# Optimization experiments

Measured on AMD Instinct MI355X. Metric: run time of the kernel, lower is better.

Reference implementation:

```python
import jax, jax.numpy as jnp
import numpy as np

# Model dims (see shape_source)
N, S, E, NMP, H, O = 20000, 16, 160000, 2, 4, 64
D_FEAT, E_DIM, PREP, NCLS, B = 64, 32, 128, 8, 4096
D1 = H * O  # 256, node/edge dim after layer 0


def setup_inputs() -> dict:
    key = jax.random.key(0)
    ks = jax.random.split(key, 24)
    g = lambda i, shape, fan: jax.random.normal(ks[i], shape, jnp.float32) * (fan ** -0.5)
    return {
        "feats": jax.random.normal(ks[0], (N, D_FEAT), jnp.float32),
        "edge_emb": jax.random.normal(ks[1], (NMP, E, E_DIM), jnp.float32),
        "W_prep0": g(2, (D_FEAT, PREP), D_FEAT),
        "W_prep1": g(3, (D_FEAT, PREP), D_FEAT),
        "edge_prep_w": g(4, (NMP, E_DIM, PREP), E_DIM),
        "edge_wq_l0": g(5, (NMP, H, PREP, O), PREP),
        "edge_wk_l0": g(6, (NMP, H, PREP, O), PREP),
        "edge_wq_l1": g(7, (NMP, H, D1, O), D1),
        "edge_wk_l1": g(8, (NMP, H, D1, O), D1),
        "node_wq_l0": g(9, (NMP, H, PREP, O), PREP),
        "node_wk_l0": g(10, (NMP, H, PREP, O), PREP),
        "node_wq_l1": g(11, (NMP, H, D1, O), D1),
        "node_wk_l1": g(12, (NMP, H, D1, O), D1),
        "Wg": g(13, (2 * D1, PREP), 2 * D1),
        "vg": g(14, (PREP,), PREP),
        "W_fc": g(15, (2 * D1, NCLS), 2 * D1),
        "b_fc": jnp.zeros((NCLS,), jnp.float32),
        "node2edge_idx": jax.random.randint(ks[20], (NMP, N, S), 0, E),
        "edge_node_adj": jax.random.randint(ks[21], (NMP, E, 2), 0, N),
        "train_ids": jax.random.randint(ks[22], (B,), 0, N),
    }


def _attn_agg(x_q, x_neigh, wq, wk):
    """Multi-head attention aggregator.
    x_q [M,d], x_neigh [M,s,d2], wq [H,d,O], wk [H,d2,O] -> [M, H*O]."""
    q = jnp.einsum('md,hdo->mho', x_q, wq)
    k = jnp.einsum('msd,hdo->msho', x_neigh, wk)
    logits = jnp.einsum('mho,msho->mhs', q, k) / np.float32(np.sqrt(O))
    a = jax.nn.softmax(logits, axis=-1)
    agg = jnp.einsum('mhs,msho->mho', a, k)
    out = jax.nn.elu(q + agg)
    return out.reshape(out.shape[0], H * O)


def reference(feats, edge_emb, W_prep0, W_prep1, edge_prep_w,
              edge_wq_l0, edge_wk_l0, edge_wq_l1, edge_wk_l1,
              node_wq_l0, node_wk_l0, node_wq_l1, node_wk_l1,
              Wg, vg, W_fc, b_fc,
              node2edge_idx, edge_node_adj, train_ids):
    e_wq, e_wk = [edge_wq_l0, edge_wq_l1], [edge_wk_l0, edge_wk_l1]
    n_wq, n_wk = [node_wq_l0, node_wq_l1], [node_wk_l0, node_wk_l1]
    outs = []
    for mp in range(NMP):  # small fixed count of message-passing branches
        dummy = feats @ W_prep0          # prep layer 0  [N,PREP]
        all_feats = feats @ W_prep1      # prep layer 1  [N,PREP]
        all_edges = edge_emb[mp] @ edge_prep_w[mp]  # [E,PREP]
        skip = []
        for l in range(2):  # depth
            # edge update: gather endpoint node feats [E,2,d], attend, concat heads
            neigh_nodes = all_feats[edge_node_adj[mp]]
            next_edges = _attn_agg(all_edges, neigh_nodes, e_wq[l][mp], e_wk[l][mp])
            # node update: gather incident edge feats [N,S,d] from OLD all_edges
            src = dummy if l == 0 else all_feats
            neigh_edges = all_edges[node2edge_idx[mp]]
            next_feats = _attn_agg(src, neigh_edges, n_wq[l][mp], n_wk[l][mp])
            skip.append(next_feats)
            all_feats, all_edges = next_feats, next_edges
        outs.append(jnp.concatenate(skip, axis=-1)[train_ids])  # [B, 2*D1]
    x = jnp.stack(outs, 0)  # [NMP, B, 512]
    # gated metapath aggregation (mp_agg): softmax over mp axis
    gate = jax.nn.softmax(jnp.einsum('mbe,e->mb', jnp.tanh(jnp.einsum('mbd,de->mbe', x, Wg)), vg), axis=0)
    pooled = jnp.einsum('mb,mbd->bd', gate, x)
    logits = pooled @ W_fc + b_fc  # [B, NCLS]
    return logits, gate
```

## Files before the change

### kernel.cpp

```cpp
#include <hip/hip_runtime.h>
#include <hip/hip_bf16.h>
#include <math.h>

#define N_NODES 20000
#define S_NE    16
#define E_EDGES 160000
#define NMP     2
#define H_HEADS 4
#define O_DIM   64
#define D_FEAT  64
#define E_DIMC  32
#define PREP    128
#define NCLS    8
#define B_TR    4096
#define D1      256
#define NSLOT   (B_TR * S_NE)

#define LDA0    132
#define LDA1    260
#define NPAD    264

typedef __hip_bfloat16 bf16;
typedef unsigned short u16;
typedef __attribute__((ext_vector_type(8))) short s8v;
typedef __attribute__((ext_vector_type(4))) float f4v;

template <typename T>
__device__ __forceinline__ float ldv(const void* p, size_t i) {
    if constexpr (sizeof(T) == 4) return ((const float*)p)[i];
    else return __bfloat162float(((const bf16*)p)[i]);
}
template <typename T>
__device__ __forceinline__ float4 ld4(const void* p, size_t i) {
    if constexpr (sizeof(T) == 4) {
        return *(const float4*)((const float*)p + i);
    } else {
        float4 r;
        r.x = ldv<T>(p, i); r.y = ldv<T>(p, i + 1);
        r.z = ldv<T>(p, i + 2); r.w = ldv<T>(p, i + 3);
        return r;
    }
}
template <typename T>
__device__ __forceinline__ void stv(void* p, size_t i, float v) {
    if constexpr (sizeof(T) == 4) ((float*)p)[i] = v;
    else ((bf16*)p)[i] = __float2bfloat16(v);
}
template <typename T>
__device__ __forceinline__ bool active(const int* flag) {
    return *flag == (sizeof(T) == 4 ? 1 : 0);
}

__device__ __forceinline__ u16 f2bf(float x) {
    bf16 h = __float2bfloat16(x);
    return *reinterpret_cast<u16*>(&h);
}
__device__ __forceinline__ float bf2f(u16 u) {
    bf16 h; *reinterpret_cast<u16*>(&h) = u;
    return __bfloat162float(h);
}
__device__ __forceinline__ void splitbf(float x, u16& h, u16& l) {
    h = f2bf(x);
    l = f2bf(x - bf2f(h));
}

__device__ __forceinline__ float wave_sum(float v) {
    #pragma unroll
    for (int off = 32; off > 0; off >>= 1) v += __shfl_xor(v, off, 64);
    return v;
}
__device__ __forceinline__ float og_sum(float v) {
    v += __shfl_xor(v, 4, 64);  v += __shfl_xor(v, 8, 64);
    v += __shfl_xor(v, 16, 64); v += __shfl_xor(v, 32, 64);
    return v;
}
__device__ __forceinline__ float grp16_sum(float v) {
    v += __shfl_xor(v, 1, 64); v += __shfl_xor(v, 2, 64);
    v += __shfl_xor(v, 4, 64); v += __shfl_xor(v, 8, 64);
    return v;
}
__device__ __forceinline__ float mg_sum(float v) {
    v += __shfl_xor(v, 1, 64); v += __shfl_xor(v, 2, 64); return v;
}
__device__ __forceinline__ float mg_max(float v) {
    v = fmaxf(v, __shfl_xor(v, 1, 64)); v = fmaxf(v, __shfl_xor(v, 2, 64)); return v;
}
__device__ __forceinline__ float eluf(float x) { return x > 0.f ? x : expf(x) - 1.f; }
__device__ __forceinline__ float4 elu4(float4 v) {
    v.x = eluf(v.x); v.y = eluf(v.y); v.z = eluf(v.z); v.w = eluf(v.w); return v;
}

#define FMA4C(acc, s, b) do { (acc).x += (s)*(b).x; (acc).y += (s)*(b).y; \
                              (acc).z += (s)*(b).z; (acc).w += (s)*(b).w; } while (0)
#define ZERO4(v) do { (v).x = 0.f; (v).y = 0.f; (v).z = 0.f; (v).w = 0.f; } while (0)

__global__ void k_detect(const unsigned* __restrict__ w, int* __restrict__ flag) {
    int t = threadIdx.x;
    int bad = 0;
    for (int i = t; i < 512; i += 64) {
        float v = __uint_as_float((w[i] & 0xffffu) << 16);
        if (!(fabsf(v) < 64.f)) bad++;
    }
    #pragma unroll
    for (int off = 32; off > 0; off >>= 1) bad += __shfl_xor(bad, off, 64);
    if (t == 0) *flag = (bad > 32) ? 1 : 0;
}

template <typename T>
__device__ void precomb2_body(const void* epw, const void* ewq, const void* nwk0,
                              const void* Wp1, const void* ewk,
                              const void* Wp0, const void* nwq0,
                              float* wkn, float* wq0,
                              u16* qeh, u16* qel, u16* k0h, u16* k0l) {
    int idx = blockIdx.x * 256 + threadIdx.x;
    if (idx >= 98304) return;
    int combo, rem;
    if (idx < 16384)      { combo = 0; rem = idx; }
    else if (idx < 32768) { combo = 1; rem = idx - 16384; }
    else if (idx < 65536) { combo = 2; rem = idx - 32768; }
    else                  { combo = 3; rem = idx - 65536; }
    int mp, r, n;
    if (combo < 2) { mp = rem >> 13; r = (rem >> 8) & 31; n = rem & 255; }
    else           { mp = rem >> 14; r = (rem >> 8) & 63; n = rem & 255; }
    int h = n >> 6, o = n & 63;
    const void* Aw; const void* Bw; size_t aoff;
    size_t boff = (size_t)mp * H_HEADS * PREP * O_DIM + (size_t)h * PREP * O_DIM + o;
    switch (combo) {
        case 0: Aw = epw; Bw = ewq;  aoff = (size_t)mp * E_DIMC * PREP + (size_t)r * PREP; break;
        case 1: Aw = epw; Bw = nwk0; aoff = (size_t)mp * E_DIMC * PREP + (size_t)r * PREP; break;
        case 2: Aw = Wp1; Bw = ewk;  aoff = (size_t)r * PREP; break;
        default:Aw = Wp0; Bw = nwq0; aoff = (size_t)r * PREP; break;
    }
    float acc = 0.f;
    #pragma unroll 4
    for (int p = 0; p < PREP; ++p)
        acc += ldv<T>(Aw, aoff + p) * ldv<T>(Bw, boff + (size_t)p * O_DIM);
    if (combo < 2) {
        u16 hh, ll; splitbf(acc, hh, ll);
        size_t dst = (size_t)mp * (256 * 32) + (size_t)n * 32 + r;
        if (combo == 0) { qeh[dst] = hh; qel[dst] = ll; }
        else            { k0h[dst] = hh; k0l[dst] = ll; }
    } else if (combo == 2) {
        wkn[(size_t)mp * 64 * D1 + (size_t)r * D1 + n] = acc;
    } else {
        wq0[(size_t)mp * 64 * D1 + (size_t)r * D1 + n] = acc;
    }
}
__global__ void k_precomb2(const void* epw, const void* ewq, const void* nwk0,
                           const void* Wp1, const void* ewk,
                           const void* Wp0, const void* nwq0,
                           float* wkn, float* wq0,
                           u16* qeh, u16* qel, u16* k0h, u16* k0l,
                           const int* flag) {
    if (*flag == 1) precomb2_body<float>(epw, ewq, nwk0, Wp1, ewk, Wp0, nwq0, wkn, wq0, qeh, qel, k0h, k0l);
    else            precomb2_body<bf16 >(epw, ewq, nwk0, Wp1, ewk, Wp0, nwq0, wkn, wq0, qeh, qel, k0h, k0l);
}

template <typename T>
__device__ void embsplit_body(const void* emb, u16* eh, u16* el) {
    size_t idx = (size_t)blockIdx.x * 256 + threadIdx.x;
    if (idx >= (size_t)NMP * E_EDGES * E_DIMC) return;
    float v = ldv<T>(emb, idx);
    u16 hh, ll; splitbf(v, hh, ll);
    eh[idx] = hh; el[idx] = ll;
}
__global__ void k_embsplit(const void* emb, u16* eh, u16* el, const int* flag) {
    if (*flag == 1) embsplit_body<float>(emb, eh, el);
    else            embsplit_body<bf16 >(emb, eh, el);
}

template <typename T>
__device__ void wt1_body(const void* wk1, const void* wq1,
                         u16* kth, u16* ktl, u16* qth, u16* qtl) {
    int idx = blockIdx.x * 256 + threadIdx.x;
    int k = idx & 255, n = (idx >> 8) & 255;
    int wsel = (idx >> 16) & 1, mp = idx >> 17;
    size_t src = (size_t)mp * (H_HEADS * D1 * O_DIM) + (size_t)(n >> 6) * (D1 * O_DIM)
               + (size_t)k * O_DIM + (n & 63);
    float v = ldv<T>(wsel ? wq1 : wk1, src);
    u16 h, l; splitbf(v, h, l);
    size_t dst = (size_t)mp * 65536 + (size_t)n * 256 + k;
    if (wsel) { qth[dst] = h; qtl[dst] = l; }
    else      { kth[dst] = h; ktl[dst] = l; }
}
__global__ void k_wt1(const void* wk1, const void* wq1,
                      u16* kth, u16* ktl, u16* qth, u16* qtl, const int* flag) {
    if (*flag == 1) wt1_body<float>(wk1, wq1, kth, ktl, qth, qtl);
    else            wt1_body<bf16 >(wk1, wq1, kth, ktl, qth, qtl);
}

template <typename T>
__device__ void wgt_body(const void* Wg, u16* gh, u16* gl) {
    int idx = blockIdx.x * 256 + threadIdx.x;
    int n = idx >> 9, k = idx & 511;
    float v = ldv<T>(Wg, (size_t)k * PREP + n);
    u16 h, l; splitbf(v, h, l);
    gh[(size_t)n * 512 + k] = h;
    gl[(size_t)n * 512 + k] = l;
}
__global__ void k_wgt(const void* Wg, u16* gh, u16* gl, const int* flag) {
    if (*flag == 1) wgt_body<float>(Wg, gh, gl);
    else            wgt_body<bf16 >(Wg, gh, gl);
}

template <typename TA, typename TB>
__device__ void gemm_body(const void* A, size_t aOff, const int* Aidx, int strideA,
                          const void* B, int sH, int sD,
                          float* C, int ldC, int M, int K) {
    int bm = blockIdx.x * 64;
    int h  = blockIdx.y;
    int t  = threadIdx.x;
    int tx = t & 15, ty = t >> 4;

    __shared__ float As[32][68];
    __shared__ float Bs[32][68];

    float acc[4][4] = {{0.f}};
    int arow = t >> 3, kq = (t & 7) * 4;
    int brow = t >> 4, nq = (t & 15) * 4;

    for (int k0 = 0; k0 < K; k0 += 32) {
        #pragma unroll
        for (int c = 0; c < 2; ++c) {
            int rm = arow + 32 * c;
            int gr = bm + rm;
            gr = (gr < M) ? gr : 0;
            size_t row = Aidx ? (size_t)Aidx[gr] : (size_t)gr;
            float4 a = ld4<TA>(A, aOff + row * strideA + k0 + kq);
            As[kq + 0][rm] = a.x; As[kq + 1][rm] = a.y;
            As[kq + 2][rm] = a.z; As[kq + 3][rm] = a.w;
        }
        #pragma unroll
        for (int c = 0; c < 2; ++c) {
            int rk = brow + 16 * c;
            float4 b = ld4<TB>(B, (size_t)h * sH + (size_t)(k0 + rk) * sD + nq);
            *(float4*)&Bs[rk][nq] = b;
        }
        __syncthreads();
        #pragma unroll
        for (int kk = 0; kk < 32; ++kk) {
            float4 av = *(const float4*)&As[kk][ty * 4];
            float4 bv = *(const float4*)&Bs[kk][tx * 4];
            float am[4] = {av.x, av.y, av.z, av.w};
            #pragma unroll
            for (int i = 0; i < 4; ++i) {
                acc[i][0] += am[i] * bv.x; acc[i][1] += am[i] * bv.y;
                acc[i][2] += am[i] * bv.z; acc[i][3] += am[i] * bv.w;
            }
        }
        __syncthreads();
    }
    #pragma unroll
    for (int i = 0; i < 4; ++i) {
        int m = bm + ty * 4 + i;
        if (m < M) {
            float4 st; st.x = acc[i][0]; st.y = acc[i][1];
            st.z = acc[i][2]; st.w = acc[i][3];
            *(float4*)&C[(size_t)m * ldC + h * 64 + tx * 4] = st;
        }
    }
}
__global__ __launch_bounds__(256) void k_gemm_rf(
        const void* A, size_t aOff, const int* Aidx, int strideA,
        const float* B, int sH, int sD, float* C, int ldC, int M, int K,
        const int* flag) {
    if (*flag == 1) gemm_body<float, float>(A, aOff, Aidx, strideA, B, sH, sD, C, ldC, M, K);
    else            gemm_body<bf16,  float>(A, aOff, Aidx, strideA, B, sH, sD, C, ldC, M, K);
}

template <int K, bool G>
__device__ __forceinline__ void mfma_core(
        const u16* __restrict__ Ah, const u16* __restrict__ Al,
        const int* __restrict__ rows,
        const u16* __restrict__ Bh, const u16* __restrict__ Bl,
        int rbase, int bn, int lane, f4v acc[4][4]) {
    int fr = lane & 15;
    int kq = (lane >> 4) * 8;
    #pragma unroll
    for (int i = 0; i < 4; ++i)
        #pragma unroll
        for (int j = 0; j < 4; ++j) acc[i][j] = f4v{0.f, 0.f, 0.f, 0.f};
    #pragma unroll 2
    for (int k0 = 0; k0 < K; k0 += 32) {
        s8v ah[4], al[4], bh[4], bl[4];
        #pragma unroll
        for (int i = 0; i < 4; ++i) {
            size_t arow;
            if constexpr (G) arow = (size_t)rows[rbase + i * 16 + fr];
            else             arow = (size_t)(rbase + i * 16 + fr);
            size_t ao = arow * K + k0 + kq;
            ah[i] = *(const s8v*)(Ah + ao);
            al[i] = *(const s8v*)(Al + ao);
            size_t bo = (size_t)(bn + i * 16 + fr) * K + k0 + kq;
            bh[i] = *(const s8v*)(Bh + bo);
            bl[i] = *(const s8v*)(Bl + bo);
        }
        #pragma unroll
        for (int i = 0; i < 4; ++i)
            #pragma unroll
            for (int j = 0; j < 4; ++j) {
                acc[i][j] = __builtin_amdgcn_mfma_f32_16x16x32_bf16(al[i], bh[j], acc[i][j], 0, 0, 0);
                acc[i][j] = __builtin_amdgcn_mfma_f32_16x16x32_bf16(ah[i], bl[j], acc[i][j], 0, 0, 0);
                acc[i][j] = __builtin_amdgcn_mfma_f32_16x16x32_bf16(ah[i], bh[j], acc[i][j], 0, 0, 0);
            }
    }
}

template <int K>
__global__ __launch_bounds__(256) void k_mfma(
        const u16* __restrict__ Ah, const u16* __restrict__ Al,
        const u16* __restrict__ Bh, const u16* __restrict__ Bl,
        float* __restrict__ C, int ldC) {
    int w = threadIdx.x >> 6, lane = threadIdx.x & 63;
    int bm = blockIdx.x * 128 + (w & 1) * 64;
    int bn = blockIdx.y * 128 + (w >> 1) * 64;
    f4v acc[4][4];
    mfma_core<K, false>(Ah, Al, nullptr, Bh, Bl, bm, bn, lane, acc);
    int cn = lane & 15, cr = (lane >> 4) * 4;
    #pragma unroll
    for (int i = 0; i < 4; ++i) {
        int m0 = bm + i * 16 + cr;
        #pragma unroll
        for (int j = 0; j < 4; ++j) {
            int n = bn + j * 16 + cn;
            #pragma unroll
            for (int r = 0; r < 4; ++r)
                C[(size_t)(m0 + r) * ldC + n] = acc[i][j][r];
        }
    }
}

template <int K, bool G>
__global__ __launch_bounds__(256) void k_mfma_nattn(
        const u16* __restrict__ Ah, const u16* __restrict__ Al,
        const int* __restrict__ rows,
        const u16* __restrict__ Bh, const u16* __restrict__ Bl,
        const float* __restrict__ q,
        u16* __restrict__ o0h, u16* __restrict__ o0l,
        float* __restrict__ xrow, int xoff,
        u16* __restrict__ xh, u16* __restrict__ xl) {
    int w = threadIdx.x >> 6, lane = threadIdx.x & 63;
    int rbase = blockIdx.x * 128 + (w & 1) * 64;
    int bn = blockIdx.y * 128 + (w >> 1) * 64;
    f4v acc[4][4];
    mfma_core<K, G>(Ah, Al, rows, Bh, Bl, rbase, bn, lane, acc);

    int cn = lane & 15, grp = lane >> 4;
    #pragma unroll
    for (int i = 0; i < 4; ++i) {
        int b = (rbase >> 4) + i;
        float qv[4];
        #pragma unroll
        for (int j = 0; j < 4; ++j)
            qv[j] = q[(size_t)b * D1 + bn + j * 16 + cn];
        float lg[4];
        #pragma unroll
        for (int r = 0; r < 4; ++r) {
            float p = 0.f;
            #pragma unroll
            for (int j = 0; j < 4; ++j) p += acc[i][j][r] * qv[j];
            lg[r] = grp16_sum(p) * 0.125f;
        }
        float mx = fmaxf(fmaxf(lg[0], lg[1]), fmaxf(lg[2], lg[3]));
        mx = fmaxf(mx, __shfl_xor(mx, 16, 64));
        mx = fmaxf(mx, __shfl_xor(mx, 32, 64));
        float e[4], s = 0.f;
        #pragma unroll
        for (int r = 0; r < 4; ++r) { e[r] = expf(lg[r] - mx); s += e[r]; }
        s += __shfl_xor(s, 16, 64);
        s += __shfl_xor(s, 32, 64);
        float inv = 1.f / s;
        #pragma unroll
        for (int j = 0; j < 4; ++j) {
            float ag = e[0] * acc[i][j][0] + e[1] * acc[i][j][1]
                     + e[2] * acc[i][j][2] + e[3] * acc[i][j][3];
            ag += __shfl_xor(ag, 16, 64);
            ag += __shfl_xor(ag, 32, 64);
            float v = eluf(qv[j] + ag * inv);
            if (grp == 0) {
                int col = bn + j * 16 + cn;
                xrow[(size_t)b * (2 * D1) + xoff + col] = v;
                u16 hh, ll; splitbf(v, hh, ll);
                xh[(size_t)b * (2 * D1) + xoff + col] = hh;
                xl[(size_t)b * (2 * D1) + xoff + col] = ll;
                if (o0h) {
                    o0h[(size_t)b * D1 + col] = hh;
                    o0l[(size_t)b * D1 + col] = ll;
                }
            }
        }
    }
}

__global__ __launch_bounds__(256) void k_mega(
        const u16* __restrict__ Ah, const u16* __restrict__ Al,
        const int* __restrict__ rows,
        const u16* __restrict__ qBh, const u16* __restrict__ qBl,
        const float* __restrict__ Kn,
        const int* __restrict__ adjA, const int* __restrict__ adjB,
        const u16* __restrict__ kBh, const u16* __restrict__ kBl,
        const float* __restrict__ q,
        float* __restrict__ xrow,
        u16* __restrict__ xh, u16* __restrict__ xl) {
    __shared__ u16 sh_[64][NPAD];
    __shared__ u16 sl_[64][NPAD];
    int w = threadIdx.x >> 6, lane = threadIdx.x & 63;
    int rbase = blockIdx.x * 64;
    int bn = w * 64;

    f4v acc[4][4];
    mfma_core<32, true>(Ah, Al, rows, qBh, qBl, rbase, bn, lane, acc);

    int cn = lane & 15, cr = (lane >> 4) * 4;
    #pragma unroll
    for (int i = 0; i < 4; ++i) {
        #pragma unroll
        for (int r = 0; r < 4; ++r) {
            int lrow = i * 16 + cr + r;
            int slot = rbase + lrow;
            size_t ra = (size_t)adjA[slot] * D1;
            size_t rb = (size_t)adjB[slot] * D1;
            float kA[4], kB[4];
            float pA = 0.f, pB = 0.f;
            #pragma unroll
            for (int j = 0; j < 4; ++j) {
                int col = bn + j * 16 + cn;
                kA[j] = Kn[ra + col];
                kB[j] = Kn[rb + col];
                pA += acc[i][j][r] * kA[j];
                pB += acc[i][j][r] * kB[j];
            }
            float lA = grp16_sum(pA) * 0.125f;
            float lB = grp16_sum(pB) * 0.125f;
            float m = fmaxf(lA, lB);
            float eA = expf(lA - m), eB = expf(lB - m);
            float inv = 1.f / (eA + eB);
            #pragma unroll
            for (int j = 0; j < 4; ++j) {
                int col = bn + j * 16 + cn;
                float v = eluf(acc[i][j][r] + (eA * kA[j] + eB * kB[j]) * inv);
                u16 hh, ll; splitbf(v, hh, ll);
                sh_[lrow][col] = hh;
                sl_[lrow][col] = ll;
            }
        }
    }
    __syncthreads();

    int fr = lane & 15, kq = (lane >> 4) * 8;
    #pragma unroll
    for (int i = 0; i < 4; ++i)
        #pragma unroll
        for (int j = 0; j < 4; ++j) acc[i][j] = f4v{0.f, 0.f, 0.f, 0.f};
    #pragma unroll 2
    for (int k0 = 0; k0 < 256; k0 += 32) {
        s8v ah[4], al[4], bh[4], bl[4];
        #pragma unroll
        for (int i = 0; i < 4; ++i) {
            int lr = i * 16 + fr;
            ah[i] = *(const s8v*)&sh_[lr][k0 + kq];
            al[i] = *(const s8v*)&sl_[lr][k0 + kq];
            size_t bo = (size_t)(bn + i * 16 + fr) * 256 + k0 + kq;
            bh[i] = *(const s8v*)(kBh + bo);
            bl[i] = *(const s8v*)(kBl + bo);
        }
        #pragma unroll
        for (int i = 0; i < 4; ++i)
            #pragma unroll
            for (int j = 0; j < 4; ++j) {
                acc[i][j] = __builtin_amdgcn_mfma_f32_16x16x32_bf16(al[i], bh[j], acc[i][j], 0, 0, 0);
                acc[i][j] = __builtin_amdgcn_mfma_f32_16x16x32_bf16(ah[i], bl[j], acc[i][j], 0, 0, 0);
                acc[i][j] = __builtin_amdgcn_mfma_f32_16x16x32_bf16(ah[i], bh[j], acc[i][j], 0, 0, 0);
            }
    }

    int grp = lane >> 4;
    #pragma unroll
    for (int i = 0; i < 4; ++i) {
        int b = (rbase >> 4) + i;
        float qv[4];
        #pragma unroll
        for (int j = 0; j < 4; ++j)
            qv[j] = q[(size_t)b * D1 + bn + j * 16 + cn];
        float lg[4];
        #pragma unroll
        for (int r = 0; r < 4; ++r) {
            float p = 0.f;
            #pragma unroll
            for (int j = 0; j < 4; ++j) p += acc[i][j][r] * qv[j];
            lg[r] = grp16_sum(p) * 0.125f;
        }
        float mx = fmaxf(fmaxf(lg[0], lg[1]), fmaxf(lg[2], lg[3]));
        mx = fmaxf(mx, __shfl_xor(mx, 16, 64));
        mx = fmaxf(mx, __shfl_xor(mx, 32, 64));
        float e[4], s = 0.f;
        #pragma unroll
        for (int r = 0; r < 4; ++r) { e[r] = expf(lg[r] - mx); s += e[r]; }
        s += __shfl_xor(s, 16, 64);
        s += __shfl_xor(s, 32, 64);
        float inv = 1.f / s;
        #pragma unroll
        for (int j = 0; j < 4; ++j) {
            float ag = e[0] * acc[i][j][0] + e[1] * acc[i][j][1]
                     + e[2] * acc[i][j][2] + e[3] * acc[i][j][3];
            ag += __shfl_xor(ag, 16, 64);
            ag += __shfl_xor(ag, 32, 64);
            float v = eluf(qv[j] + ag * inv);
            if (grp == 0) {
                int col = bn + j * 16 + cn;
                xrow[(size_t)b * (2 * D1) + D1 + col] = v;
                u16 hh, ll; splitbf(v, hh, ll);
                xh[(size_t)b * (2 * D1) + D1 + col] = hh;
                xl[(size_t)b * (2 * D1) + D1 + col] = ll;
            }
        }
    }
}

__global__ void k_slot_setup(const int* __restrict__ n2e_mp,
                             const int* __restrict__ adj_mp,
                             const int* __restrict__ tid,
                             int* __restrict__ eid,
                             int* __restrict__ adjA,
                             int* __restrict__ adjB) {
    int i = blockIdx.x * blockDim.x + threadIdx.x;
    if (i >= NSLOT) return;
    int b = i >> 4, s = i & 15;
    int e = n2e_mp[(size_t)tid[b] * S_NE + s];
    eid[i] = e;
    adjA[i] = adj_mp[(size_t)e * 2 + 0];
    adjB[i] = adj_mp[(size_t)e * 2 + 1];
}

template <typename T>
__device__ void gate_fin_body(const float* gmat, const void* vg, float* gate_pre) {
    int row = blockIdx.x;
    int t = threadIdx.x;
    float v = tanhf(gmat[(size_t)row * PREP + t]) * ldv<T>(vg, t);
    __shared__ float red[128];
    red[t] = v;
    __syncthreads();
    for (int s = 64; s > 0; s >>= 1) { if (t < s) red[t] += red[t + s]; __syncthreads(); }
    if (t == 0) gate_pre[row] = red[0];
}
__global__ void k_gate_fin(const float* gmat, const void* vg, float* gate_pre,
                           const int* flag) {
    if (*flag == 1) gate_fin_body<float>(gmat, vg, gate_pre);
    else            gate_fin_body<bf16 >(gmat, vg, gate_pre);
}

template <typename T>
__device__ void gate_dir_body(const float* xcat, const void* Wg, const void* vg,
                              float* gate_pre) {
    int mb = blockIdx.x;
    int t = threadIdx.x;
    __shared__ float xr[2 * D1];
    for (int idx = t; idx < 2 * D1; idx += 128) xr[idx] = xcat[(size_t)mb * (2 * D1) + idx];
    __syncthreads();
    float acc = 0.f;
    for (int d = 0; d < 2 * D1; ++d) acc += xr[d] * ldv<T>(Wg, (size_t)d * PREP + t);
    float gp = tanhf(acc) * ldv<T>(vg, t);
    __shared__ float red[128];
    red[t] = gp;
    __syncthreads();
    for (int s = 64; s > 0; s >>= 1) { if (t < s) red[t] += red[t + s]; __syncthreads(); }
    if (t == 0) gate_pre[mb] = red[0];
}
__global__ void k_gate_direct(const float* xcat, const void* Wg, const void* vg,
                              float* gate_pre, const int* flag) {
    if (*flag == 1) gate_dir_body<float>(xcat, Wg, vg, gate_pre);
    else            gate_dir_body<bf16 >(xcat, Wg, vg, gate_pre);
}

template <typename T>
__device__ void final_body(const float* xcat, const float* gate_pre,
                           const void* Wfc, const void* bfc, void* out) {
    int b = blockIdx.x;
    int t = threadIdx.x;
    float g0 = gate_pre[b], g1 = gate_pre[B_TR + b];
    float mx = fmaxf(g0, g1);
    float e0 = expf(g0 - mx), e1 = expf(g1 - mx);
    float inv = 1.f / (e0 + e1);
    float w0 = e0 * inv, w1 = e1 * inv;
    __shared__ float pooled[2 * D1];
    for (int d = t; d < 2 * D1; d += 64)
        pooled[d] = w0 * xcat[(size_t)b * (2 * D1) + d]
                  + w1 * xcat[(size_t)(B_TR + b) * (2 * D1) + d];
    __syncthreads();
    if (t < NCLS) {
        float acc = ldv<T>(bfc, t);
        for (int d = 0; d < 2 * D1; ++d) acc += pooled[d] * ldv<T>(Wfc, (size_t)d * NCLS + t);
        stv<T>(out, (size_t)b * NCLS + t, acc);
    }
    if (t == 8) stv<T>(out, (size_t)B_TR * NCLS + b, w0);
    if (t == 9) stv<T>(out, (size_t)B_TR * NCLS + B_TR + b, w1);
}
__global__ void k_final(const float* xcat, const float* gate_pre,
                        const void* Wfc, const void* bfc, void* out,
                        const int* flag) {
    if (*flag == 1) final_body<float>(xcat, gate_pre, Wfc, bfc, out);
    else            final_body<bf16 >(xcat, gate_pre, Wfc, bfc, out);
}

template <typename T>
__global__ void k_prep_nodes(const void* __restrict__ feats,
                             const void* __restrict__ W,
                             float* __restrict__ out,
                             const int* __restrict__ flag) {
    if (!active<T>(flag)) return;
    int g = blockIdx.x * blockDim.x + threadIdx.x;
    if (g >= N_NODES * 32) return;
    int n = g >> 5, pg = g & 31;
    float4 acc; ZERO4(acc);
    #pragma unroll 8
    for (int d = 0; d < D_FEAT; ++d) {
        float f = ldv<T>(feats, (size_t)n * D_FEAT + d);
        float4 w4 = ld4<T>(W, (size_t)d * PREP + pg * 4);
        FMA4C(acc, f, w4);
    }
    *(float4*)(out + (size_t)n * PREP + pg * 4) = acc;
}

template <typename T>
__global__ __launch_bounds__(256) void k_fused(
        const void* __restrict__ feats,
        const void* __restrict__ edge_emb_mp,
        const void* __restrict__ W_prep0,
        const void* __restrict__ epw_mp,
        const void* __restrict__ ewq,
        const void* __restrict__ ewk,
        const void* __restrict__ nwq0,
        const void* __restrict__ nwk0,
        const void* __restrict__ nwq1,
        const void* __restrict__ nwk1,
        const int*  __restrict__ n2e_mp,
        const int*  __restrict__ adj_mp,
        const int*  __restrict__ tid,
        const float* __restrict__ all_feats0,
        float* __restrict__ xcat_mp,
        const int* __restrict__ flag) {
    if (!active<T>(flag)) return;
    int b = blockIdx.x;
    int t = threadIdx.x;
    int h = t >> 6;
    int lane = t & 63;
    int mg = lane & 3, og = lane >> 2;

    __shared__ int   s_eid[S_NE];
    __shared__ int   s_nrow[2 * S_NE];
    __shared__ __align__(16) float s_emb[S_NE * E_DIMC];
    __shared__ __align__(16) float s_f[D_FEAT];
    __shared__ __align__(16) float s_q0[PREP];
    __shared__ __align__(16) float s_eprep[S_NE * LDA0];
    __shared__ __align__(16) float s_xn_pool[2 * S_NE * LDA0];
    __shared__ __align__(16) float s_out0[D1];
    float* s_nedge = s_xn_pool;

    int tid_b = tid[b];
    if (t < S_NE)   s_eid[t] = n2e_mp[(size_t)tid_b * S_NE + t];
    if (t < D_FEAT) s_f[t] = ldv<T>(feats, (size_t)tid_b * D_FEAT + t);
    __syncthreads();

    if (t < 2 * S_NE) s_nrow[t] = adj_mp[(size_t)s_eid[t >> 1] * 2 + (t & 1)];
    {
        int j = t, s = j >> 5, d = j & 31;
        s_emb[j] = ldv<T>(edge_emb_mp, (size_t)s_eid[s] * E_DIMC + d);
        j = t + 256; s = j >> 5; d = j & 31;
        s_emb[j] = ldv<T>(edge_emb_mp, (size_t)s_eid[s] * E_DIMC + d);
    }
    if (t < PREP) {
        float a = 0.f;
        #pragma unroll
        for (int d = 0; d < D_FEAT; ++d) a += s_f[d] * ldv<T>(W_prep0, d * PREP + t);
        s_q0[t] = a;
    }
    __syncthreads();

    #pragma unroll
    for (int k = 0; k < 4; ++k) {
        int j = t + 256 * k;
        int r = j >> 5, dc = j & 31;
        float4 v = *(const float4*)(all_feats0 + (size_t)s_nrow[r] * PREP + dc * 4);
        *(float4*)&s_xn_pool[r * LDA0 + dc * 4] = v;
    }
    {
        int s = t >> 4, pg = t & 15;
        float4 a0, a1; ZERO4(a0); ZERO4(a1);
        #pragma unroll
        for (int d = 0; d < E_DIMC; ++d) {
            float e = s_emb[s * E_DIMC + d];
            float4 w0 = ld4<T>(epw_mp, (size_t)d * PREP + pg * 8);
            float4 w1 = ld4<T>(epw_mp, (size_t)d * PREP + pg * 8 + 4);
            FMA4C(a0, e, w0); FMA4C(a1, e, w1);
        }
        *(float4*)&s_eprep[s * LDA0 + pg * 8]     = a0;
        *(float4*)&s_eprep[s * LDA0 + pg * 8 + 4] = a1;
    }
    __syncthreads();

    float4 aq[4], ak[8];
    #pragma unroll
    for (int i = 0; i < 4; ++i) ZERO4(aq[i]);
    #pragma unroll
    for (int i = 0; i < 8; ++i) ZERO4(ak[i]);
    {
        size_t wb = (size_t)h * PREP * O_DIM + og * 4;
        for (int kk = 0; kk < PREP; kk += 4) {
            float4 bq[4], bk[4];
            #pragma unroll
            for (int j = 0; j < 4; ++j) {
                bq[j] = ld4<T>(ewq, wb + (size_t)(kk + j) * O_DIM);
                bk[j] = ld4<T>(ewk, wb + (size_t)(kk + j) * O_DIM);
            }
            #pragma unroll
            for (int i = 0; i < 4; ++i) {
                float4 a = *(const float4*)&s_eprep[(mg + 4 * i) * LDA0 + kk];
                FMA4C(aq[i], a.x, bq[0]); FMA4C(aq[i], a.y, bq[1]);
                FMA4C(aq[i], a.z, bq[2]); FMA4C(aq[i], a.w, bq[3]);
            }
            #pragma unroll
            for (int i = 0; i < 8; ++i) {
                int r = 2 * mg + (i & 1) + 8 * (i >> 1);
                float4 a = *(const float4*)&s_xn_pool[r * LDA0 + kk];
                FMA4C(ak[i], a.x, bk[0]); FMA4C(ak[i], a.y, bk[1]);
                FMA4C(ak[i], a.z, bk[2]); FMA4C(ak[i], a.w, bk[3]);
            }
        }
    }
    __syncthreads();

    #pragma unroll
    for (int j = 0; j < 4; ++j) {
        int s = mg + 4 * j;
        float4 q = aq[j], kA = ak[2 * j], kB = ak[2 * j + 1];
        float lA = og_sum(q.x * kA.x + q.y * kA.y + q.z * kA.z + q.w * kA.w) * 0.125f;
        float lB = og_sum(q.x * kB.x + q.y * kB.y + q.z * kB.z + q.w * kB.w) * 0.125f;
        float m = fmaxf(lA, lB);
        float eA = expf(lA - m), eB = expf(lB - m);
        float inv = 1.f / (eA + eB);
        float4 v;
        v.x = q.x + (eA * kA.x + eB * kB.x) * inv;
        v.y = q.y + (eA * kA.y + eB * kB.y) * inv;
        v.z = q.z + (eA * kA.z + eB * kB.z) * inv;
        v.w = q.w + (eA * kA.w + eB * kB.w) * inv;
        *(float4*)&s_nedge[s * LDA1 + h * O_DIM + og * 4] = elu4(v);
    }

    float4 zq; ZERO4(zq);
    float4 zk[4];
    #pragma unroll
    for (int i = 0; i < 4; ++i) ZERO4(zk[i]);
    {
        size_t wb = (size_t)h * PREP * O_DIM + og * 4;
        for (int kk = 0; kk < PREP; kk += 4) {
            float4 q4 = *(const float4*)&s_q0[kk];
            float4 bq[4], bk[4];
            #pragma unroll
            for (int j = 0; j < 4; ++j) {
                bq[j] = ld4<T>(nwq0, wb + (size_t)(kk + j) * O_DIM);
                bk[j] = ld4<T>(nwk0, wb + (size_t)(kk + j) * O_DIM);
            }
            FMA4C(zq, q4.x, bq[0]); FMA4C(zq, q4.y, bq[1]);
            FMA4C(zq, q4.z, bq[2]); FMA4C(zq, q4.w, bq[3]);
            #pragma unroll
            for (int i = 0; i < 4; ++i) {
                float4 a = *(const float4*)&s_eprep[(mg + 4 * i) * LDA0 + kk];
                FMA4C(zk[i], a.x, bk[0]); FMA4C(zk[i], a.y, bk[1]);
                FMA4C(zk[i], a.z, bk[2]); FMA4C(zk[i], a.w, bk[3]);
            }
        }
    }
    {
        float lg[4];
        #pragma unroll
        for (int j = 0; j < 4; ++j)
            lg[j] = og_sum(zq.x * zk[j].x + zq.y * zk[j].y +
                           zq.z * zk[j].z + zq.w * zk[j].w) * 0.125f;
        float mx = fmaxf(fmaxf(lg[0], lg[1]), fmaxf(lg[2], lg[3]));
        mx = mg_max(mx);
        float ea[4], ssum = 0.f;
        #pragma unroll
        for (int j = 0; j < 4; ++j) { ea[j] = expf(lg[j] - mx); ssum += ea[j]; }
        ssum = mg_sum(ssum);
        float inv = 1.f / ssum;
        float4 part; ZERO4(part);
        #pragma unroll
        for (int j = 0; j < 4; ++j) FMA4C(part, ea[j], zk[j]);
        part.x = mg_sum(part.x); part.y = mg_sum(part.y);
        part.z = mg_sum(part.z); part.w = mg_sum(part.w);
        float4 v;
        v.x = zq.x + part.x * inv; v.y = zq.y + part.y * inv;
        v.z = zq.z + part.z * inv; v.w = zq.w + part.w * inv;
        v = elu4(v);
        if (mg == 0) {
            *(float4*)&s_out0[h * O_DIM + og * 4] = v;
            *(float4*)(xcat_mp + (size_t)b * (2 * D1) + h * O_DIM + og * 4) = v;
        }
    }
    __syncthreads();

    ZERO4(zq);
    #pragma unroll
    for (int i = 0; i < 4; ++i) ZERO4(zk[i]);
    {
        size_t wb = (size_t)h * D1 * O_DIM + og * 4;
        for (int kk = 0; kk < D1; kk += 4) {
            float4 q4 = *(const float4*)&s_out0[kk];
            float4 bq[4], bk[4];
            #pragma unroll
            for (int j = 0; j < 4; ++j) {
                bq[j] = ld4<T>(nwq1, wb + (size_t)(kk + j) * O_DIM);
                bk[j] = ld4<T>(nwk1, wb + (size_t)(kk + j) * O_DIM);
            }
            FMA4C(zq, q4.x, bq[0]); FMA4C(zq, q4.y, bq[1]);
            FMA4C(zq, q4.z, bq[2]); FMA4C(zq, q4.w, bq[3]);
            #pragma unroll
            for (int i = 0; i < 4; ++i) {
                float4 a = *(const float4*)&s_nedge[(mg + 4 * i) * LDA1 + kk];
                FMA4C(zk[i], a.x, bk[0]); FMA4C(zk[i], a.y, bk[1]);
                FMA4C(zk[i], a.z, bk[2]); FMA4C(zk[i], a.w, bk[3]);
            }
        }
    }
    {
        float lg[4];
        #pragma unroll
        for (int j = 0; j < 4; ++j)
            lg[j] = og_sum(zq.x * zk[j].x + zq.y * zk[j].y +
                           zq.z * zk[j].z + zq.w * zk[j].w) * 0.125f;
        float mx = fmaxf(fmaxf(lg[0], lg[1]), fmaxf(lg[2], lg[3]));
        mx = mg_max(mx);
        float ea[4], ssum = 0.f;
        #pragma unroll
        for (int j = 0; j < 4; ++j) { ea[j] = expf(lg[j] - mx); ssum += ea[j]; }
        ssum = mg_sum(ssum);
        float inv = 1.f / ssum;
        float4 part; ZERO4(part);
        #pragma unroll
        for (int j = 0; j < 4; ++j) FMA4C(part, ea[j], zk[j]);
        part.x = mg_sum(part.x); part.y = mg_sum(part.y);
        part.z = mg_sum(part.z); part.w = mg_sum(part.w);
        float4 v;
        v.x = zq.x + part.x * inv; v.y = zq.y + part.y * inv;
        v.z = zq.z + part.z * inv; v.w = zq.w + part.w * inv;
        v = elu4(v);
        if (mg == 0)
            *(float4*)(xcat_mp + (size_t)b * (2 * D1) + D1 + h * O_DIM + og * 4) = v;
    }
}

extern "C" void kernel_launch(void* const* d_in, const int* in_sizes, int n_in,
                              void* d_out, int out_size, void* d_ws, size_t ws_size,
                              hipStream_t stream) {
    const void* feats       = d_in[0];
    const void* edge_emb    = d_in[1];
    const void* W_prep0     = d_in[2];
    const void* W_prep1     = d_in[3];
    const void* edge_prep_w = d_in[4];
    const void* e_wq0       = d_in[5];
    const void* e_wk0       = d_in[6];
    const void* n_wq0       = d_in[9];
    const void* n_wk0       = d_in[10];
    const void* n_wq1       = d_in[11];
    const void* n_wk1       = d_in[12];
    const void* Wg          = d_in[13];
    const void* vg          = d_in[14];
    const void* Wfc         = d_in[15];
    const void* bfc         = d_in[16];
    const int*  n2e         = (const int*)d_in[17];
    const int*  adj         = (const int*)d_in[18];
    const int*  tid         = (const int*)d_in[19];

    float* ws   = (float*)d_ws;
    int*   flag = (int*)ws;
    float* base = ws + 4;
    size_t avail = (ws_size >= 16) ? (ws_size - 16) / 4 : 0;

    k_detect<<<1, 64, 0, stream>>>((const unsigned*)feats, flag);

    size_t off = 0;
    auto alloc = [&](size_t n) { size_t o = off; off += (n + 3) & ~(size_t)3; return o; };
    size_t o_xcat = alloc((size_t)NMP * B_TR * 2 * D1);
    size_t o_gmat = alloc((size_t)NMP * B_TR * PREP);
    size_t o_gpre = alloc(NMP * B_TR);
    size_t o_wkn  = alloc(NMP * 64 * D1);
    size_t o_wq0  = alloc(NMP * 64 * D1);
    size_t o_qeh  = alloc(NMP * 256 * 32 / 2);
    size_t o_qel  = alloc(NMP * 256 * 32 / 2);
    size_t o_k0h  = alloc(NMP * 256 * 32 / 2);
    size_t o_k0l  = alloc(NMP * 256 * 32 / 2);
    size_t o_ebh  = alloc((size_t)NMP * E_EDGES * E_DIMC / 2);
    size_t o_ebl  = alloc((size_t)NMP * E_EDGES * E_DIMC / 2);
    size_t o_Kn   = alloc((size_t)N_NODES * D1);
    size_t o_q0   = alloc((size_t)B_TR * D1);
    size_t o_Q1   = alloc((size_t)B_TR * D1);
    size_t o_eid  = alloc(NSLOT);
    size_t o_adjA = alloc(NSLOT);
    size_t o_adjB = alloc(NSLOT);
    size_t o_o0h  = alloc((size_t)B_TR * D1 / 2);
    size_t o_o0l  = alloc((size_t)B_TR * D1 / 2);
    size_t o_xh   = alloc((size_t)NMP * B_TR * D1);
    size_t o_xl   = alloc((size_t)NMP * B_TR * D1);
    size_t o_wk1h = alloc((size_t)NMP * 32768);
    size_t o_wk1l = alloc((size_t)NMP * 32768);
    size_t o_wq1h = alloc((size_t)NMP * 32768);
    size_t o_wq1l = alloc((size_t)NMP * 32768);
    size_t o_wgh  = alloc(32768);
    size_t o_wgl  = alloc(32768);
    size_t fixed = off;

    int CH = (fixed <= avail) ? B_TR : 0;

    if (CH > 0) {
        float* xcat = base + o_xcat;
        float* gmat = base + o_gmat;
        float* gpre = base + o_gpre;
        float* wkn  = base + o_wkn;
        float* wq0  = base + o_wq0;
        u16*   qeh  = (u16*)(base + o_qeh);
        u16*   qel  = (u16*)(base + o_qel);
        u16*   k0h  = (u16*)(base + o_k0h);
        u16*   k0l  = (u16*)(base + o_k0l);
        u16*   ebh  = (u16*)(base + o_ebh);
        u16*   ebl  = (u16*)(base + o_ebl);
        float* Kn   = base + o_Kn;
        float* q0   = base + o_q0;
        float* Q1   = base + o_Q1;
        int*   eid  = (int*)(base + o_eid);
        int*   adjA = (int*)(base + o_adjA);
        int*   adjB = (int*)(base + o_adjB);
        u16*   o0h  = (u16*)(base + o_o0h);
        u16*   o0l  = (u16*)(base + o_o0l);
        u16*   xh   = (u16*)(base + o_xh);
        u16*   xl   = (u16*)(base + o_xl);
        u16*   wk1h = (u16*)(base + o_wk1h);
        u16*   wk1l = (u16*)(base + o_wk1l);
        u16*   wq1h = (u16*)(base + o_wq1h);
        u16*   wq1l = (u16*)(base + o_wq1l);
        u16*   wgh  = (u16*)(base + o_wgh);
        u16*   wgl  = (u16*)(base + o_wgl);
        int NC = B_TR / CH;

        k_precomb2<<<384, 256, 0, stream>>>(edge_prep_w, e_wq0, n_wk0, W_prep1,
                                            e_wk0, W_prep0, n_wq0,
                                            wkn, wq0, qeh, qel, k0h, k0l, flag);
        k_embsplit<<<(NMP * E_EDGES * E_DIMC + 255) / 256, 256, 0, stream>>>(
            edge_emb, ebh, ebl, flag);
        k_wt1<<<1024, 256, 0, stream>>>(n_wk1, n_wq1, wk1h, wk1l, wq1h, wq1l, flag);
        k_wgt<<<256, 256, 0, stream>>>(Wg, wgh, wgl, flag);

        for (int mp = 0; mp < NMP; ++mp) {
            k_slot_setup<<<(NSLOT + 255) / 256, 256, 0, stream>>>(
                n2e + (size_t)mp * N_NODES * S_NE,
                adj + (size_t)mp * E_EDGES * 2,
                tid, eid, adjA, adjB);

            k_gemm_rf<<<dim3((N_NODES + 63) / 64, 4), 256, 0, stream>>>(
                feats, 0, nullptr, D_FEAT, wkn + (size_t)mp * 64 * D1,
                64, D1, Kn, D1, N_NODES, D_FEAT, flag);
            k_gemm_rf<<<dim3(B_TR / 64, 4), 256, 0, stream>>>(
                feats, 0, tid, D_FEAT, wq0 + (size_t)mp * 64 * D1,
                64, D1, q0, D1, B_TR, D_FEAT, flag);

            const u16* ebh_mp = ebh + (size_t)mp * E_EDGES * E_DIMC;
            const u16* ebl_mp = ebl + (size_t)mp * E_EDGES * E_DIMC;

            for (int c = 0; c < NC; ++c) {
                int c0 = c * CH;
                int MS = CH * S_NE;
                k_mfma_nattn<32, true><<<dim3(MS / 128, 2), 256, 0, stream>>>(
                    ebh_mp, ebl_mp, eid + (size_t)c0 * S_NE,
                    k0h + (size_t)mp * 8192, k0l + (size_t)mp * 8192,
                    q0 + (size_t)c0 * D1, o0h, o0l,
                    xcat + ((size_t)mp * B_TR + c0) * 2 * D1, 0,
                    xh + ((size_t)mp * B_TR + c0) * 2 * D1,
                    xl + ((size_t)mp * B_TR + c0) * 2 * D1);
                k_mfma<256><<<dim3(CH / 128, 2), 256, 0, stream>>>(
                    o0h, o0l, wq1h + (size_t)mp * 65536, wq1l + (size_t)mp * 65536,
                    Q1, D1);
                k_mega<<<MS / 64, 256, 0, stream>>>(
                    ebh_mp, ebl_mp, eid + (size_t)c0 * S_NE,
                    qeh + (size_t)mp * 8192, qel + (size_t)mp * 8192,
                    Kn, adjA + (size_t)c0 * S_NE, adjB + (size_t)c0 * S_NE,
                    wk1h + (size_t)mp * 65536, wk1l + (size_t)mp * 65536,
                    Q1,
                    xcat + ((size_t)mp * B_TR + c0) * 2 * D1,
                    xh + ((size_t)mp * B_TR + c0) * 2 * D1,
                    xl + ((size_t)mp * B_TR + c0) * 2 * D1);
            }
        }
        k_mfma<512><<<dim3(NMP * B_TR / 128, 1), 256, 0, stream>>>(
            xh, xl, wgh, wgl, gmat, PREP);
        k_gate_fin<<<NMP * B_TR, 128, 0, stream>>>(gmat, vg, gpre, flag);
        k_final<<<B_TR, 64, 0, stream>>>(xcat, gpre, Wfc, bfc, d_out, flag);
    } else {
        size_t f_off = 0;
        auto falloc = [&](size_t n) { size_t o = f_off; f_off += (n + 3) & ~(size_t)3; return o; };
        float* af0  = base + falloc((size_t)N_NODES * PREP);
        float* xcat = base + falloc((size_t)NMP * B_TR * 2 * D1);
        float* gpre = base + falloc(NMP * B_TR);

        k_prep_nodes<float><<<(N_NODES * 32 + 255) / 256, 256, 0, stream>>>(
            feats, W_prep1, af0, flag);
        k_prep_nodes<bf16><<<(N_NODES * 32 + 255) / 256, 256, 0, stream>>>(
            feats, W_prep1, af0, flag);

        for (int mp = 0; mp < NMP; ++mp) {
            #define FUSED_ARGS(esz)                                                   \
                feats,                                                                \
                (const char*)edge_emb + (esz) * (size_t)mp * E_EDGES * E_DIMC,        \
                W_prep0,                                                              \
                (const char*)edge_prep_w + (esz) * (size_t)mp * E_DIMC * PREP,        \
                (const char*)e_wq0 + (esz) * (size_t)mp * H_HEADS * PREP * O_DIM,     \
                (const char*)e_wk0 + (esz) * (size_t)mp * H_HEADS * PREP * O_DIM,     \
                (const char*)n_wq0 + (esz) * (size_t)mp * H_HEADS * PREP * O_DIM,     \
                (const char*)n_wk0 + (esz) * (size_t)mp * H_HEADS * PREP * O_DIM,     \
                (const char*)n_wq1 + (esz) * (size_t)mp * H_HEADS * D1 * O_DIM,       \
                (const char*)n_wk1 + (esz) * (size_t)mp * H_HEADS * D1 * O_DIM,       \
                n2e + (size_t)mp * N_NODES * S_NE,                                    \
                adj + (size_t)mp * E_EDGES * 2,                                       \
                tid, af0, xcat + (size_t)mp * B_TR * 2 * D1, flag
            k_fused<float><<<B_TR, 256, 0, stream>>>(FUSED_ARGS(4));
            k_fused<bf16><<<B_TR, 256, 0, stream>>>(FUSED_ARGS(2));
            #undef FUSED_ARGS
        }
        k_gate_direct<<<NMP * B_TR, 128, 0, stream>>>(xcat, Wg, vg, gpre, flag);
        k_final<<<B_TR, 64, 0, stream>>>(xcat, gpre, Wfc, bfc, d_out, flag);
    }
}
```

Measured before the change: 513.9 us.

## Split k_mega across 8 waves with 32-row tiles and inline first GEMM

k_mega now launches 512 threads per block, so each wave handles a 32x64 tile instead of a 64x64 tile. The accumulator array shrinks from 4x4 to 2x4, and the first GEMM is inlined instead of calling mfma_core. Adjacency indices are loaded before the MFMA so their latency can overlap with the matrix work. The aim is lower register pressure and more waves in flight to hide the gather latency, at the cost of each wave reloading the B operand for its half of the rows.

```diff
diff --git a/kernel.cpp b/kernel.cpp
--- a/kernel.cpp
+++ b/kernel.cpp
@@ -392,7 +392,7 @@
     }
 }
 
-__global__ __launch_bounds__(256) void k_mega(
+__global__ __launch_bounds__(512, 4) void k_mega(
         const u16* __restrict__ Ah, const u16* __restrict__ Al,
         const int* __restrict__ rows,
         const u16* __restrict__ qBh, const u16* __restrict__ qBl,
@@ -405,21 +405,59 @@
     __shared__ u16 sh_[64][NPAD];
     __shared__ u16 sl_[64][NPAD];
     int w = threadIdx.x >> 6, lane = threadIdx.x & 63;
-    int rbase = blockIdx.x * 64;
-    int bn = w * 64;
-
-    f4v acc[4][4];
-    mfma_core<32, true>(Ah, Al, rows, qBh, qBl, rbase, bn, lane, acc);
-
+    int wr = w & 1, wc = w >> 1;
+    int blk = blockIdx.x * 64;
+    int rbase = blk + wr * 32;
+    int bn = wc * 64;
+    int fr = lane & 15, kq = (lane >> 4) * 8;
     int cn = lane & 15, cr = (lane >> 4) * 4;
-    #pragma unroll
-    for (int i = 0; i < 4; ++i) {
+
+    int raA[2][4], raB[2][4];
+    #pragma unroll
+    for (int i = 0; i < 2; ++i)
         #pragma unroll
         for (int r = 0; r < 4; ++r) {
-            int lrow = i * 16 + cr + r;
-            int slot = rbase + lrow;
-            size_t ra = (size_t)adjA[slot] * D1;
-            size_t rb = (size_t)adjB[slot] * D1;
+            int slot = rbase + i * 16 + cr + r;
+            raA[i][r] = adjA[slot] * D1;
+            raB[i][r] = adjB[slot] * D1;
+        }
+
+    f4v acc[2][4];
+    #pragma unroll
+    for (int i = 0; i < 2; ++i)
+        #pragma unroll
+        for (int j = 0; j < 4; ++j) acc[i][j] = f4v{0.f, 0.f, 0.f, 0.f};
+    {
+        s8v ah[2], al[2], bh[4], bl[4];
+        #pragma unroll
+        for (int i = 0; i < 2; ++i) {
+            size_t ao = (size_t)rows[rbase + i * 16 + fr] * E_DIMC + kq;
+            ah[i] = *(const s8v*)(Ah + ao);
+            al[i] = *(const s8v*)(Al + ao);
+        }
+        #pragma unroll
+        for (int j = 0; j < 4; ++j) {
+            size_t bo = (size_t)(bn + j * 16 + fr) * E_DIMC + kq;
+            bh[j] = *(const s8v*)(qBh + bo);
+            bl[j] = *(const s8v*)(qBl + bo);
+        }
+        #pragma unroll
+        for (int i = 0; i < 2; ++i)
+            #pragma unroll
+            for (int j = 0; j < 4; ++j) {
+                acc[i][j] = __builtin_amdgcn_mfma_f32_16x16x32_bf16(al[i], bh[j], acc[i][j], 0, 0, 0);
+                acc[i][j] = __builtin_amdgcn_mfma_f32_16x16x32_bf16(ah[i], bl[j], acc[i][j], 0, 0, 0);
+                acc[i][j] = __builtin_amdgcn_mfma_f32_16x16x32_bf16(ah[i], bh[j], acc[i][j], 0, 0, 0);
+            }
+    }
+
+    #pragma unroll
+    for (int i = 0; i < 2; ++i) {
+        #pragma unroll
+        for (int r = 0; r < 4; ++r) {
+            int lrow = wr * 32 + i * 16 + cr + r;
+            size_t ra = (size_t)raA[i][r];
+            size_t rb = (size_t)raB[i][r];
             float kA[4], kB[4];
             float pA = 0.f, pB = 0.f;
             #pragma unroll
@@ -447,25 +485,27 @@
     }
     __syncthreads();
 
-    int fr = lane & 15, kq = (lane >> 4) * 8;
-    #pragma unroll
-    for (int i = 0; i < 4; ++i)
+    #pragma unroll
+    for (int i = 0; i < 2; ++i)
         #pragma unroll
         for (int j = 0; j < 4; ++j) acc[i][j] = f4v{0.f, 0.f, 0.f, 0.f};
     #pragma unroll 2
     for (int k0 = 0; k0 < 256; k0 += 32) {
-        s8v ah[4], al[4], bh[4], bl[4];
-        #pragma unroll
-        for (int i = 0; i < 4; ++i) {
-            int lr = i * 16 + fr;
+        s8v ah[2], al[2], bh[4], bl[4];
+        #pragma unroll
+        for (int i = 0; i < 2; ++i) {
+            int lr = wr * 32 + i * 16 + fr;
             ah[i] = *(const s8v*)&sh_[lr][k0 + kq];
             al[i] = *(const s8v*)&sl_[lr][k0 + kq];
-            size_t bo = (size_t)(bn + i * 16 + fr) * 256 + k0 + kq;
-            bh[i] = *(const s8v*)(kBh + bo);
-            bl[i] = *(const s8v*)(kBl + bo);
-        }
-        #pragma unroll
-        for (int i = 0; i < 4; ++i)
+        }
+        #pragma unroll
+        for (int j = 0; j < 4; ++j) {
+            size_t bo = (size_t)(bn + j * 16 + fr) * 256 + k0 + kq;
+            bh[j] = *(const s8v*)(kBh + bo);
+            bl[j] = *(const s8v*)(kBl + bo);
+        }
+        #pragma unroll
+        for (int i = 0; i < 2; ++i)
             #pragma unroll
             for (int j = 0; j < 4; ++j) {
                 acc[i][j] = __builtin_amdgcn_mfma_f32_16x16x32_bf16(al[i], bh[j], acc[i][j], 0, 0, 0);
@@ -476,7 +516,7 @@
 
     int grp = lane >> 4;
     #pragma unroll
-    for (int i = 0; i < 4; ++i) {
+    for (int i = 0; i < 2; ++i) {
         int b = (rbase >> 4) + i;
         float qv[4];
         #pragma unroll
@@ -978,7 +1018,7 @@
                 k_mfma<256><<<dim3(CH / 128, 2), 256, 0, stream>>>(
                     o0h, o0l, wq1h + (size_t)mp * 65536, wq1l + (size_t)mp * 65536,
                     Q1, D1);
-                k_mega<<<MS / 64, 256, 0, stream>>>(
+                k_mega<<<MS / 64, 512, 0, stream>>>(
                     ebh_mp, ebl_mp, eid + (size_t)c0 * S_NE,
                     qeh + (size_t)mp * 8192, qel + (size_t)mp * 8192,
                     Kn, adjA + (size_t)c0 * S_NE, adjB + (size_t)c0 * S_NE,
```

After: 528.9 us. 1.03x slower.
